# Performance work log

Hardware: AMD Instinct MI355X
Metric: run time of the kernel (lower is better)

The kernel has to match this reference:

```python
import jax, jax.numpy as jnp
import numpy as np

N, E, B, D, L = 100000, 600000, 128, 128, 3
BOT = 64
EPS = 1e-5


def _forward(query_x, corpus_x, gin_eps, mlp_W1, mlp_b1, mlp_W2, mlp_b2, bn_gamma, bn_beta,
             pool_G1, pool_g1b, pool_G2, pool_g2b, pool_Wm,
             int_G1, int_g1b, int_G2, int_g2b, int_F1, int_f1b, int_F2, int_f2b,
             sc_G1, sc_g1b, sc_G2, sc_g2b, sc_F1, sc_f1b, sc_F2, sc_f2b,
             query_edge_index, query_graph_idx, corpus_edge_index, corpus_graph_idx, num_graphs):
    def gin(x, ei, l):
        # GINConv: sum of source-node features into targets, plus (1+eps)*self
        agg = jax.ops.segment_sum(x[ei[0]], ei[1], num_segments=x.shape[0])
        h = (1.0 + gin_eps[l]) * x + agg
        h = jax.nn.relu(h @ mlp_W1[l] + mlp_b1[l]) @ mlp_W2[l] + mlp_b2[l]
        mu = h.mean(axis=0)
        var = ((h - mu) ** 2).mean(axis=0)  # biased var (BatchNorm training mode)
        h = (h - mu) * jax.lax.rsqrt(var + EPS) * bn_gamma[l] + bn_beta[l]
        return jax.nn.relu(h)  # dropout p=0.0

    def pool(x, gidx, l):
        coef = jnp.tanh(jax.nn.relu(x @ pool_G1[l] + pool_g1b[l]) @ pool_G2[l] + pool_g2b[l])
        s = (coef + 1.0) * x
        sums = jax.ops.segment_sum(s, gidx, num_segments=num_graphs)
        cnt = jax.ops.segment_sum(jnp.ones((x.shape[0],), x.dtype), gidx, num_segments=num_graphs)
        mean = sums / cnt[:, None]
        gc = jnp.tanh(mean @ pool_Wm[l])  # [B, D]
        node_coef = jax.nn.sigmoid(jnp.sum(s * gc[gidx], axis=1))  # [N]
        return jax.ops.segment_sum(node_coef[:, None] * s, gidx, num_segments=num_graphs)

    def interact(q, c, l):
        comb = jnp.concatenate([q, c], axis=1)  # [B, 2D]
        coef = jax.nn.sigmoid(jax.nn.relu(comb @ int_G1[l] + int_g1b[l]) @ int_G2[l] + int_g2b[l])
        sc = (coef + 1.0) * comb
        return jax.nn.relu(jax.nn.relu(sc @ int_F1[l] + int_f1b[l]) @ int_F2[l] + int_f2b[l])

    qx, cx = query_x, corpus_x
    feats = []
    for l in range(gin_eps.shape[0]):
        qx = gin(qx, query_edge_index, l)
        cx = gin(cx, corpus_edge_index, l)
        feats.append(interact(pool(qx, query_graph_idx, l), pool(cx, corpus_graph_idx, l), l))
    f = jnp.concatenate(feats, axis=1)  # [B, sum(filters)//2]
    coef = jax.nn.sigmoid(jax.nn.relu(f @ sc_G1 + sc_g1b) @ sc_G2 + sc_g2b)
    sf = (coef + 1.0) * f
    return (jax.nn.relu(sf @ sc_F1 + sc_f1b) @ sc_F2 + sc_f2b).squeeze(-1)  # [B]


def setup_inputs() -> dict:
    key = jax.random.key(0)
    kit = iter(jax.random.split(key, 64))
    def nrm(shape, s=0.05):
        return jax.random.normal(next(kit), shape, jnp.float32) * s
    C, R, OUT, AGG, RG = 2 * D, (2 * D) // 4, D // 2, (3 * D) // 2, ((3 * D) // 2) // 4
    inp = {
        "query_x": nrm((N, D), 1.0),
        "query_edge_index": jax.random.randint(next(kit), (2, E), 0, N),
        "query_graph_idx": jnp.sort(jax.random.randint(next(kit), (N,), 0, B)),
        "corpus_x": nrm((N, D), 1.0),
        "corpus_edge_index": jax.random.randint(next(kit), (2, E), 0, N),
        "corpus_graph_idx": jnp.sort(jax.random.randint(next(kit), (N,), 0, B)),
        "num_graphs": B,
        "gin_eps": jnp.zeros((L,), jnp.float32),
        "mlp_W1": nrm((L, D, D)), "mlp_b1": jnp.zeros((L, D)),
        "mlp_W2": nrm((L, D, D)), "mlp_b2": jnp.zeros((L, D)),
        "bn_gamma": jnp.ones((L, D)), "bn_beta": jnp.zeros((L, D)),
        "pool_G1": nrm((L, D, D // 4)), "pool_g1b": jnp.zeros((L, D // 4)),
        "pool_G2": nrm((L, D // 4, D)), "pool_g2b": jnp.zeros((L, D)),
        "pool_Wm": nrm((L, D, D)),
        "int_G1": nrm((L, C, R)), "int_g1b": jnp.zeros((L, R)),
        "int_G2": nrm((L, R, C)), "int_g2b": jnp.zeros((L, C)),
        "int_F1": nrm((L, C, C)), "int_f1b": jnp.zeros((L, C)),
        "int_F2": nrm((L, C, OUT)), "int_f2b": jnp.zeros((L, OUT)),
        "sc_G1": nrm((AGG, RG)), "sc_g1b": jnp.zeros((RG,)),
        "sc_G2": nrm((RG, AGG)), "sc_g2b": jnp.zeros((AGG,)),
        "sc_F1": nrm((AGG, BOT)), "sc_f1b": jnp.zeros((BOT,)),
        "sc_F2": nrm((BOT, 1)), "sc_f2b": jnp.zeros((1,)),
    }
    return inp


def reference(query_x, query_edge_index, query_graph_idx, corpus_x, corpus_edge_index, corpus_graph_idx,
              num_graphs, gin_eps, mlp_W1, mlp_b1, mlp_W2, mlp_b2, bn_gamma, bn_beta,
              pool_G1, pool_g1b, pool_G2, pool_g2b, pool_Wm,
              int_G1, int_g1b, int_G2, int_g2b, int_F1, int_f1b, int_F2, int_f2b,
              sc_G1, sc_g1b, sc_G2, sc_g2b, sc_F1, sc_f1b, sc_F2, sc_f2b):
    return _forward(query_x, corpus_x, gin_eps, mlp_W1, mlp_b1, mlp_W2, mlp_b2, bn_gamma, bn_beta,
                    pool_G1, pool_g1b, pool_G2, pool_g2b, pool_Wm,
                    int_G1, int_g1b, int_G2, int_g2b, int_F1, int_f1b, int_F2, int_f2b,
                    sc_G1, sc_g1b, sc_G2, sc_g2b, sc_F1, sc_f1b, sc_F2, sc_f2b,
                    query_edge_index, query_graph_idx, corpus_edge_index, corpus_graph_idx, num_graphs)
```

## Files before the change

kernel.cpp:

```cpp
#include <hip/hip_runtime.h>
#include <hip/hip_bf16.h>

constexpr int NN  = 100000;
constexpr int NN2 = 200000;
constexpr int NE  = 600000;
constexpr int NB  = 128;
constexpr int D   = 128;
constexpr int NL  = 3;
constexpr int CAP = 48;
constexpr int MT_TOT = NN2 / 16;
constexpr int MT_Q   = NN / 16;

typedef __bf16 bf16x8 __attribute__((ext_vector_type(8)));
typedef float f32x4 __attribute__((ext_vector_type(4)));
typedef unsigned short us8 __attribute__((ext_vector_type(8)));

__device__ __forceinline__ float sigmoidf_(float x) { return 1.0f / (1.0f + __expf(-x)); }
__device__ __forceinline__ unsigned short f2b(float f) {
    __hip_bfloat16 h = __float2bfloat16(f);
    return __builtin_bit_cast(unsigned short, h);
}
__device__ __forceinline__ float b2f(unsigned short u) {
    __hip_bfloat16 h = __builtin_bit_cast(__hip_bfloat16, u);
    return __bfloat162float(h);
}
__device__ __forceinline__ bf16x8 ldfrag(const unsigned short* p) {
    return __builtin_bit_cast(bf16x8, *(const us8*)p);
}

__global__ __launch_bounds__(256) void k_csr_fill(const int* __restrict__ ei, int* __restrict__ deg,
                                                  int* __restrict__ bucket, int off) {
    int e = blockIdx.x * 256 + threadIdx.x;
    if (e < NE) {
        int src = ei[e] + off;
        int dst = ei[NE + e] + off;
        int pos = atomicAdd(&deg[dst], 1);
        if (pos < CAP) bucket[(size_t)dst * CAP + pos] = src;
    }
}

__global__ __launch_bounds__(256) void k_wprep_all(
    const float* mW1, const float* mW2, const float* pG1, const float* pG2,
    const float* iG1, const float* iG2, const float* iF1, const float* iF2,
    const float* sG1, const float* sG2, const float* sF1,
    unsigned short* W1t, unsigned short* W2t, unsigned short* G1t, unsigned short* G2t,
    unsigned short* iG1t, unsigned short* iG2t, unsigned short* iF1t, unsigned short* iF2t,
    unsigned short* sG1t, unsigned short* sG2t, unsigned short* sF1t) {
    int i = blockIdx.x * 256 + threadIdx.x;
#define SEG(CNT, KK, NN_, SRC, DST)                                              \
    if (i < (CNT)) {                                                             \
        int l = i / ((KK) * (NN_)), r = i % ((KK) * (NN_));                      \
        int n = r / (KK), k = r % (KK);                                          \
        DST[i] = f2b(SRC[(size_t)l * (KK) * (NN_) + (size_t)k * (NN_) + n]);     \
        return;                                                                  \
    }                                                                            \
    i -= (CNT);
    SEG(49152, 128, 128, mW1, W1t)
    SEG(49152, 128, 128, mW2, W2t)
    SEG(12288, 128, 32, pG1, G1t)
    SEG(12288, 32, 128, pG2, G2t)
    SEG(49152, 256, 64, iG1, iG1t)
    SEG(49152, 64, 256, iG2, iG2t)
    SEG(196608, 256, 256, iF1, iF1t)
    SEG(49152, 256, 64, iF2, iF2t)
    SEG(9216, 192, 48, sG1, sG1t)
    if (i < 12288) {
        int n = i / 64, k = i % 64;
        sG2t[i] = (k < 48) ? f2b(sG2[(size_t)k * 192 + n]) : (unsigned short)0;
        return;
    }
    i -= 12288;
    SEG(12288, 192, 64, sF1, sF1t)
#undef SEG
}

template <bool BF16IN>
__global__ __launch_bounds__(256) void k_gather(const float* __restrict__ qx, const float* __restrict__ cx,
                                                const unsigned short* __restrict__ xb, unsigned short* __restrict__ z,
                                                const int* __restrict__ deg, const int* __restrict__ bucket,
                                                const float* __restrict__ eps_p, int l) {
    int r = blockIdx.x * 16 + (threadIdx.x >> 4);
    int c8 = threadIdx.x & 15;
    float e = 1.0f + eps_p[l];
    float a[8];
    const float* base = nullptr; int off = 0;
    if constexpr (BF16IN) {
        us8 v = *(const us8*)(xb + (size_t)r * D + c8 * 8);
#pragma unroll
        for (int j = 0; j < 8; ++j) a[j] = e * b2f(v[j]);
    } else {
        base = (r < NN) ? qx : cx; off = (r < NN) ? 0 : NN;
        float4 v0 = *(const float4*)(base + (size_t)(r - off) * D + c8 * 8);
        float4 v1 = *(const float4*)(base + (size_t)(r - off) * D + c8 * 8 + 4);
        a[0] = e * v0.x; a[1] = e * v0.y; a[2] = e * v0.z; a[3] = e * v0.w;
        a[4] = e * v1.x; a[5] = e * v1.y; a[6] = e * v1.z; a[7] = e * v1.w;
    }
    int d = deg[r]; d = (d < CAP) ? d : CAP;
    const int* bk = bucket + (size_t)r * CAP;
    int i = 0;
    for (; i + 4 <= d; i += 4) {
        int s0 = bk[i], s1 = bk[i + 1], s2 = bk[i + 2], s3 = bk[i + 3];
        if constexpr (BF16IN) {
            us8 u0 = *(const us8*)(xb + (size_t)s0 * D + c8 * 8);
            us8 u1 = *(const us8*)(xb + (size_t)s1 * D + c8 * 8);
            us8 u2 = *(const us8*)(xb + (size_t)s2 * D + c8 * 8);
            us8 u3 = *(const us8*)(xb + (size_t)s3 * D + c8 * 8);
#pragma unroll
            for (int j = 0; j < 8; ++j)
                a[j] += b2f(u0[j]) + b2f(u1[j]) + b2f(u2[j]) + b2f(u3[j]);
        } else {
            const float* p0 = base + (size_t)(s0 - off) * D + c8 * 8;
            const float* p1 = base + (size_t)(s1 - off) * D + c8 * 8;
            const float* p2 = base + (size_t)(s2 - off) * D + c8 * 8;
            const float* p3 = base + (size_t)(s3 - off) * D + c8 * 8;
            float4 w0 = *(const float4*)p0, w0b = *(const float4*)(p0 + 4);
            float4 w1 = *(const float4*)p1, w1b = *(const float4*)(p1 + 4);
            float4 w2 = *(const float4*)p2, w2b = *(const float4*)(p2 + 4);
            float4 w3 = *(const float4*)p3, w3b = *(const float4*)(p3 + 4);
            a[0] += w0.x + w1.x + w2.x + w3.x; a[1] += w0.y + w1.y + w2.y + w3.y;
            a[2] += w0.z + w1.z + w2.z + w3.z; a[3] += w0.w + w1.w + w2.w + w3.w;
            a[4] += w0b.x + w1b.x + w2b.x + w3b.x; a[5] += w0b.y + w1b.y + w2b.y + w3b.y;
            a[6] += w0b.z + w1b.z + w2b.z + w3b.z; a[7] += w0b.w + w1b.w + w2b.w + w3b.w;
        }
    }
    for (; i < d; ++i) {
        int s0 = bk[i];
        if constexpr (BF16IN) {
            us8 u0 = *(const us8*)(xb + (size_t)s0 * D + c8 * 8);
#pragma unroll
            for (int j = 0; j < 8; ++j) a[j] += b2f(u0[j]);
        } else {
            const float* p0 = base + (size_t)(s0 - off) * D + c8 * 8;
            float4 w0 = *(const float4*)p0, w0b = *(const float4*)(p0 + 4);
            a[0] += w0.x; a[1] += w0.y; a[2] += w0.z; a[3] += w0.w;
            a[4] += w0b.x; a[5] += w0b.y; a[6] += w0b.z; a[7] += w0b.w;
        }
    }
    us8 o;
#pragma unroll
    for (int j = 0; j < 8; ++j) o[j] = f2b(a[j]);
    *(us8*)(z + (size_t)r * D + c8 * 8) = o;
}

constexpr int HSTR = 136;
__global__ __launch_bounds__(256, 2) void k_mlp(unsigned short* zh,
                                                const unsigned short* __restrict__ W1t,
                                                const unsigned short* __restrict__ W2t,
                                                const float* __restrict__ b1,
                                                const float* __restrict__ b2,
                                                float* __restrict__ stat) {
    __shared__ unsigned short hb[2][2][16 * HSTR];
    __shared__ float red[512];
    int wave = threadIdx.x >> 6, lane = threadIdx.x & 63;
    int col16 = lane & 15, quad = lane >> 4;
    int g = wave >> 1, half = wave & 1;
    bf16x8 bf1[4][4], bf2[4][4];
    float bb1[4], bb2[4];
#pragma unroll
    for (int t = 0; t < 4; ++t) {
        int c = half * 64 + t * 16 + col16;
        bb1[t] = b1[c]; bb2[t] = b2[c];
#pragma unroll
        for (int kc = 0; kc < 4; ++kc) {
            bf1[t][kc] = ldfrag(W1t + (size_t)c * D + kc * 32 + quad * 8);
            bf2[t][kc] = ldfrag(W2t + (size_t)c * D + kc * 32 + quad * 8);
        }
    }
    float cs[2][4] = {{0.f,0.f,0.f,0.f},{0.f,0.f,0.f,0.f}};
    float cq[2][4] = {{0.f,0.f,0.f,0.f},{0.f,0.f,0.f,0.f}};
    int groups = gridDim.x * 2;
    int iters = (MT_TOT + groups - 1) / groups;
    for (int n = 0; n < iters; ++n) {
        int mt = blockIdx.x * 2 + g + n * groups;
        bool act = (mt < MT_TOT);
        int pp = n & 1;
        unsigned short* hbuf = hb[pp][g];
        {
            const unsigned short* Ap = zh + ((size_t)(act ? mt : 0) * 16 + col16) * D + quad * 8;
            f32x4 acc[4];
#pragma unroll
            for (int t = 0; t < 4; ++t) acc[t] = (f32x4){0.f, 0.f, 0.f, 0.f};
#pragma unroll
            for (int kc = 0; kc < 4; ++kc) {
                bf16x8 af = ldfrag(Ap + kc * 32);
#pragma unroll
                for (int t = 0; t < 4; ++t)
                    acc[t] = __builtin_amdgcn_mfma_f32_16x16x32_bf16(af, bf1[t][kc], acc[t], 0, 0, 0);
            }
#pragma unroll
            for (int t = 0; t < 4; ++t) {
                int c = half * 64 + t * 16 + col16;
#pragma unroll
                for (int r = 0; r < 4; ++r)
                    hbuf[(quad * 4 + r) * HSTR + c] = f2b(fmaxf(acc[t][r] + bb1[t], 0.f));
            }
        }
        __syncthreads();
        {
            f32x4 acc[4];
#pragma unroll
            for (int t = 0; t < 4; ++t) acc[t] = (f32x4){0.f, 0.f, 0.f, 0.f};
#pragma unroll
            for (int kc = 0; kc < 4; ++kc) {
                bf16x8 af = ldfrag(&hbuf[col16 * HSTR + kc * 32 + quad * 8]);
#pragma unroll
                for (int t = 0; t < 4; ++t)
                    acc[t] = __builtin_amdgcn_mfma_f32_16x16x32_bf16(af, bf2[t][kc], acc[t], 0, 0, 0);
            }
            if (act) {
                int side = (mt < MT_Q) ? 0 : 1;
#pragma unroll
                for (int t = 0; t < 4; ++t) {
                    int c = half * 64 + t * 16 + col16;
#pragma unroll
                    for (int r = 0; r < 4; ++r) {
                        int m = mt * 16 + quad * 4 + r;
                        float v = acc[t][r] + bb2[t];
                        zh[(size_t)m * D + c] = f2b(v);
                        cs[side][t] += v; cq[side][t] += v * v;
                    }
                }
            }
        }
    }
    for (int i = threadIdx.x; i < 512; i += 256) red[i] = 0.f;
    __syncthreads();
#pragma unroll
    for (int t = 0; t < 4; ++t) {
        int c = half * 64 + t * 16 + col16;
#pragma unroll
        for (int side = 0; side < 2; ++side) {
            atomicAdd(&red[side * 256 + c], cs[side][t]);
            atomicAdd(&red[side * 256 + 128 + c], cq[side][t]);
        }
    }
    __syncthreads();
    for (int i = threadIdx.x; i < 512; i += 256) atomicAdd(&stat[i], red[i]);
}

__global__ __launch_bounds__(256, 2) void k_pool(const unsigned short* __restrict__ H,
                                                 const unsigned short* __restrict__ G1t,
                                                 const unsigned short* __restrict__ G2t,
                                                 const float* __restrict__ b1,
                                                 const float* __restrict__ b2,
                                                 const float* __restrict__ stat,
                                                 const float* __restrict__ gamma,
                                                 const float* __restrict__ beta,
                                                 unsigned short* __restrict__ Xo,
                                                 unsigned short* __restrict__ S) {
    __shared__ float sc_s[256], sh_s[256];
    __shared__ unsigned short xt[4][16 * HSTR];
    __shared__ unsigned short t2t[4][16 * 40];
    {
        int t = threadIdx.x, side = t >> 7, c = t & 127;
        const float invN = 1.0f / (float)NN;
        float mu = stat[side * 256 + c] * invN;
        float var = fmaxf(stat[side * 256 + 128 + c] * invN - mu * mu, 0.f);
        float inv = rsqrtf(var + 1e-5f);
        float s = gamma[c] * inv;
        sc_s[t] = s;
        sh_s[t] = beta[c] - mu * s;
    }
    __syncthreads();
    int wave = threadIdx.x >> 6, lane = threadIdx.x & 63;
    int col16 = lane & 15, quad = lane >> 4;
    unsigned short* xtile = xt[wave];
    unsigned short* t2tile = t2t[wave];
    bf16x8 g1f[2][4], g2f[8];
    float bb1[2], bb2[8];
#pragma unroll
    for (int t = 0; t < 2; ++t) {
        int c = t * 16 + col16;
        bb1[t] = b1[c];
#pragma unroll
        for (int kc = 0; kc < 4; ++kc)
            g1f[t][kc] = ldfrag(G1t + (size_t)c * D + kc * 32 + quad * 8);
    }
#pragma unroll
    for (int t = 0; t < 8; ++t) {
        int c = t * 16 + col16;
        bb2[t] = b2[c];
        g2f[t] = ldfrag(G2t + (size_t)c * 32 + quad * 8);
    }
    for (int mt = blockIdx.x * 4 + wave; mt < MT_TOT; mt += gridDim.x * 4) {
        int side = (mt < MT_Q) ? 0 : 1;
        const float* scp = sc_s + side * 128;
        const float* shp = sh_s + side * 128;
        const unsigned short* Hp = H + ((size_t)mt * 16 + col16) * D + quad * 8;
        unsigned short* Xp = Xo + ((size_t)mt * 16 + col16) * D + quad * 8;
        f32x4 acc1[2];
#pragma unroll
        for (int t = 0; t < 2; ++t) acc1[t] = (f32x4){0.f, 0.f, 0.f, 0.f};
#pragma unroll
        for (int kc = 0; kc < 4; ++kc) {
            us8 hv = *(const us8*)(Hp + kc * 32);
            int k0 = kc * 32 + quad * 8;
            float4 s0 = *(const float4*)&scp[k0], s1 = *(const float4*)&scp[k0 + 4];
            float4 h0 = *(const float4*)&shp[k0], h1 = *(const float4*)&shp[k0 + 4];
            us8 xv;
            xv[0] = f2b(fmaxf(b2f(hv[0]) * s0.x + h0.x, 0.f));
            xv[1] = f2b(fmaxf(b2f(hv[1]) * s0.y + h0.y, 0.f));
            xv[2] = f2b(fmaxf(b2f(hv[2]) * s0.z + h0.z, 0.f));
            xv[3] = f2b(fmaxf(b2f(hv[3]) * s0.w + h0.w, 0.f));
            xv[4] = f2b(fmaxf(b2f(hv[4]) * s1.x + h1.x, 0.f));
            xv[5] = f2b(fmaxf(b2f(hv[5]) * s1.y + h1.y, 0.f));
            xv[6] = f2b(fmaxf(b2f(hv[6]) * s1.z + h1.z, 0.f));
            xv[7] = f2b(fmaxf(b2f(hv[7]) * s1.w + h1.w, 0.f));
            *(us8*)(Xp + kc * 32) = xv;
            *(us8*)(xtile + col16 * HSTR + k0) = xv;
            bf16x8 af = __builtin_bit_cast(bf16x8, xv);
#pragma unroll
            for (int t = 0; t < 2; ++t)
                acc1[t] = __builtin_amdgcn_mfma_f32_16x16x32_bf16(af, g1f[t][kc], acc1[t], 0, 0, 0);
        }
#pragma unroll
        for (int t = 0; t < 2; ++t) {
            int c = t * 16 + col16;
#pragma unroll
            for (int r = 0; r < 4; ++r)
                t2tile[(quad * 4 + r) * 40 + c] = f2b(fmaxf(acc1[t][r] + bb1[t], 0.f));
        }
        bf16x8 af2 = ldfrag(t2tile + col16 * 40 + quad * 8);
        f32x4 acc2[8];
#pragma unroll
        for (int t = 0; t < 8; ++t) {
            acc2[t] = (f32x4){0.f, 0.f, 0.f, 0.f};
            acc2[t] = __builtin_amdgcn_mfma_f32_16x16x32_bf16(af2, g2f[t], acc2[t], 0, 0, 0);
        }
#pragma unroll
        for (int t = 0; t < 8; ++t) {
            int c = t * 16 + col16;
#pragma unroll
            for (int r = 0; r < 4; ++r) {
                int mrow = quad * 4 + r;
                float v = tanhf(acc2[t][r] + bb2[t]) + 1.f;
                S[((size_t)mt * 16 + mrow) * D + c] = f2b(v * b2f(xtile[mrow * HSTR + c]));
            }
        }
    }
}

__global__ __launch_bounds__(256) void k_segsum(const unsigned short* __restrict__ S,
                                                const int* __restrict__ gq, const int* __restrict__ gc,
                                                float* __restrict__ dst, float* __restrict__ cnt) {
    int c = threadIdx.x & (D - 1);
    int sub = threadIdx.x >> 7;
    int per = (NN2 + gridDim.x - 1) / gridDim.x;
    int r0 = blockIdx.x * per;
    int r1 = min(r0 + per, NN2);
    int r = r0 + sub;
    if (r >= r1) return;
    float acc = 0.f, cn = 0.f;
    int cur = (r < NN) ? gq[r] : 128 + gc[r - NN];
    for (; r < r1; r += 2) {
        int g = (r < NN) ? gq[r] : 128 + gc[r - NN];
        if (g != cur) {
            atomicAdd(&dst[cur * D + c], acc);
            if (c == 0) atomicAdd(&cnt[cur], cn);
            acc = 0.f; cn = 0.f; cur = g;
        }
        acc += b2f(S[(size_t)r * D + c]);
        cn += 1.f;
    }
    atomicAdd(&dst[cur * D + c], acc);
    if (c == 0) atomicAdd(&cnt[cur], cn);
}

__global__ void k_gc(const float* __restrict__ sums, const float* __restrict__ cnt,
                     const float* __restrict__ Wm, float* __restrict__ gc) {
    __shared__ float m[D];
    int b = blockIdx.x, j = threadIdx.x;
    m[j] = sums[b * D + j] / cnt[b];
    __syncthreads();
    float a = 0.f;
#pragma unroll 8
    for (int i = 0; i < D; ++i) a += m[i] * Wm[i * D + j];
    gc[b * D + j] = tanhf(a);
}

__global__ __launch_bounds__(256) void k_ncseg(const unsigned short* __restrict__ S,
                                               const int* __restrict__ gq, const int* __restrict__ gc,
                                               const float* __restrict__ gcb,
                                               float* __restrict__ dq, float* __restrict__ dc) {
    int stream = blockIdx.x * 4 + (threadIdx.x >> 6);
    int lane = threadIdx.x & 63;
    int nstream = gridDim.x * 4;
    int per = (NN2 + nstream - 1) / nstream;
    int r0 = stream * per;
    int r1 = min(r0 + per, NN2);
    if (r0 >= r1) return;
    float a0 = 0.f, a1 = 0.f;
    int cur = (r0 < NN) ? gq[r0] : 128 + gc[r0 - NN];
    for (int r = r0; r < r1; ++r) {
        int g = (r < NN) ? gq[r] : 128 + gc[r - NN];
        if (g != cur) {
            float* base = (cur < 128) ? (dq + cur * D) : (dc + (cur - 128) * D);
            atomicAdd(&base[lane * 2], a0);
            atomicAdd(&base[lane * 2 + 1], a1);
            a0 = 0.f; a1 = 0.f; cur = g;
        }
        ushort2 sv = *(const ushort2*)&S[(size_t)r * D + lane * 2];
        float2 gv = *(const float2*)&gcb[(size_t)g * D + lane * 2];
        float v0 = b2f(sv.x), v1 = b2f(sv.y);
        float p = v0 * gv.x + v1 * gv.y;
#pragma unroll
        for (int off = 1; off < 64; off <<= 1) p += __shfl_xor(p, off, 64);
        float nc = sigmoidf_(p);
        a0 += nc * v0; a1 += nc * v1;
    }
    float* base = (cur < 128) ? (dq + cur * D) : (dc + (cur - 128) * D);
    atomicAdd(&base[lane * 2], a0);
    atomicAdd(&base[lane * 2 + 1], a1);
}

constexpr int LSTR = 264;
__global__ __launch_bounds__(256) void k_interact(const float* __restrict__ pooled,
                                                  const unsigned short* __restrict__ iG1t, const float* __restrict__ ig1b,
                                                  const unsigned short* __restrict__ iG2t, const float* __restrict__ ig2b,
                                                  const unsigned short* __restrict__ iF1t, const float* __restrict__ if1b,
                                                  const unsigned short* __restrict__ iF2t, const float* __restrict__ if2b,
                                                  unsigned short* __restrict__ featsb) {
    __shared__ unsigned short bufC[16 * LSTR];
    __shared__ unsigned short bufA[16 * LSTR];
    __shared__ unsigned short bufB[16 * LSTR];
    int t = threadIdx.x, wave = t >> 6, lane = t & 63;
    int col16 = lane & 15, quad = lane >> 4;
    int pg = blockIdx.x & 7, l = blockIdx.x >> 3;
    int p0 = pg * 16;
    {
        int r = t >> 4, c0 = (t & 15) * 16;
        const float* src = (c0 < 128)
            ? (pooled + (size_t)l * NB * D + (size_t)(p0 + r) * D + c0)
            : (pooled + (size_t)(NL + l) * NB * D + (size_t)(p0 + r) * D + (c0 - 128));
#pragma unroll
        for (int j = 0; j < 16; ++j) bufC[r * LSTR + c0 + j] = f2b(src[j]);
    }
    __syncthreads();
    {
        f32x4 acc = (f32x4){0.f, 0.f, 0.f, 0.f};
        int n = wave * 16 + col16;
#pragma unroll
        for (int kc = 0; kc < 8; ++kc) {
            bf16x8 af = ldfrag(&bufC[col16 * LSTR + kc * 32 + quad * 8]);
            bf16x8 bfr = ldfrag(iG1t + ((size_t)l * 64 + n) * 256 + kc * 32 + quad * 8);
            acc = __builtin_amdgcn_mfma_f32_16x16x32_bf16(af, bfr, acc, 0, 0, 0);
        }
        float bb = ig1b[(size_t)l * 64 + n];
#pragma unroll
// ... 116 lines not shown
            bf16x8 af = ldfrag(&bufA[col16 * LSTR + kc * 32 + quad * 8]);
#pragma unroll
            for (int tt = 0; tt < 3; ++tt) {
                int n = wave * 48 + tt * 16 + col16;
                bf16x8 bfr = ldfrag(sG2t + (size_t)n * 64 + kc * 32 + quad * 8);
                acc[tt] = __builtin_amdgcn_mfma_f32_16x16x32_bf16(af, bfr, acc[tt], 0, 0, 0);
            }
        }
#pragma unroll
        for (int tt = 0; tt < 3; ++tt) {
            int n = wave * 48 + tt * 16 + col16;
            float bb = sg2b[n];
#pragma unroll
            for (int r = 0; r < 4; ++r) {
                int row = quad * 4 + r;
                float s = (sigmoidf_(acc[tt][r] + bb) + 1.f) * b2f(bufF[row * 200 + n]);
                bufB[row * LSTR + n] = f2b(s);
            }
        }
    }
    __syncthreads();
    {
        f32x4 acc = (f32x4){0.f, 0.f, 0.f, 0.f};
        int n = wave * 16 + col16;
#pragma unroll
        for (int kc = 0; kc < 6; ++kc) {
            bf16x8 af = ldfrag(&bufB[col16 * LSTR + kc * 32 + quad * 8]);
            bf16x8 bfr = ldfrag(sF1t + (size_t)n * 192 + kc * 32 + quad * 8);
            acc = __builtin_amdgcn_mfma_f32_16x16x32_bf16(af, bfr, acc, 0, 0, 0);
        }
        float bb = sf1b[n], w2 = sF2[n];
#pragma unroll
        for (int r = 0; r < 4; ++r)
            redf[(quad * 4 + r) * 65 + n] = fmaxf(acc[r] + bb, 0.f) * w2;
    }
    __syncthreads();
    if (t < 16) {
        float s = 0.f;
#pragma unroll 8
        for (int i = 0; i < 64; ++i) s += redf[t * 65 + i];
        out[p0 + t] = s + sf2b[0];
    }
}

extern "C" void kernel_launch(void* const* d_in, const int* in_sizes, int n_in,
                              void* d_out, int out_size, void* d_ws, size_t ws_size,
                              hipStream_t stream) {
    const float* query_x   = (const float*)d_in[0];
    const int*   query_ei  = (const int*)d_in[1];
    const int*   query_gi  = (const int*)d_in[2];
    const float* corpus_x  = (const float*)d_in[3];
    const int*   corpus_ei = (const int*)d_in[4];
    const int*   corpus_gi = (const int*)d_in[5];
    const float* gin_eps   = (const float*)d_in[7];
    const float* mlp_W1    = (const float*)d_in[8];
    const float* mlp_b1    = (const float*)d_in[9];
    const float* mlp_W2    = (const float*)d_in[10];
    const float* mlp_b2    = (const float*)d_in[11];
    const float* bn_gamma  = (const float*)d_in[12];
    const float* bn_beta   = (const float*)d_in[13];
    const float* pool_G1   = (const float*)d_in[14];
    const float* pool_g1b  = (const float*)d_in[15];
    const float* pool_G2   = (const float*)d_in[16];
    const float* pool_g2b  = (const float*)d_in[17];
    const float* pool_Wm   = (const float*)d_in[18];
    const float* int_G1    = (const float*)d_in[19];
    const float* int_g1b   = (const float*)d_in[20];
    const float* int_G2    = (const float*)d_in[21];
    const float* int_g2b   = (const float*)d_in[22];
    const float* int_F1    = (const float*)d_in[23];
    const float* int_f1b   = (const float*)d_in[24];
    const float* int_F2    = (const float*)d_in[25];
    const float* int_f2b   = (const float*)d_in[26];
    const float* sc_G1     = (const float*)d_in[27];
    const float* sc_g1b    = (const float*)d_in[28];
    const float* sc_G2     = (const float*)d_in[29];
    const float* sc_g2b    = (const float*)d_in[30];
    const float* sc_F1     = (const float*)d_in[31];
    const float* sc_f1b    = (const float*)d_in[32];
    const float* sc_F2     = (const float*)d_in[33];
    const float* sc_f2b    = (const float*)d_in[34];
    float* out = (float*)d_out;

    unsigned short* Zb  = (unsigned short*)d_ws;
    unsigned short* Xb  = Zb + (size_t)NN2 * D;
    unsigned short* Sb  = Xb + (size_t)NN2 * D;
    unsigned short* featsb = Sb + (size_t)NN2 * D;
    unsigned short* W1t = featsb + 128 * 192;
    unsigned short* W2t = W1t + NL * D * D;
    unsigned short* G1t = W2t + NL * D * D;
    unsigned short* G2t = G1t + NL * 32 * D;
    unsigned short* iG1t = G2t + NL * D * 32;
    unsigned short* iG2t = iG1t + NL * 64 * 256;
    unsigned short* iF1t = iG2t + NL * 256 * 64;
    unsigned short* iF2t = iF1t + NL * 256 * 256;
    unsigned short* sG1t = iF2t + NL * 64 * 256;
    unsigned short* sG2t = sG1t + 48 * 192;
    unsigned short* sF1t = sG2t + 192 * 64;
    int* deg    = (int*)(sF1t + 64 * 192);
    int* bucket = deg + NN2;
    float* bn_stat  = (float*)(bucket + (size_t)NN2 * CAP);
    float* seg_sum  = bn_stat + NL * 512;
    float* seg_cnt  = seg_sum + 256 * D;
    float* gcb      = seg_cnt + 256;
    float* pooled   = gcb + 256 * D;

    k_wprep_all<<<1956, 256, 0, stream>>>(mlp_W1, mlp_W2, pool_G1, pool_G2,
                                          int_G1, int_G2, int_F1, int_F2,
                                          sc_G1, sc_G2, sc_F1,
                                          W1t, W2t, G1t, G2t, iG1t, iG2t, iF1t, iF2t,
                                          sG1t, sG2t, sF1t);

    hipMemsetAsync(deg, 0, NN2 * sizeof(int), stream);
    hipMemsetAsync(bn_stat, 0, NL * 512 * sizeof(float), stream);
    hipMemsetAsync(pooled, 0, 2 * NL * NB * D * sizeof(float), stream);
    k_csr_fill<<<(NE + 255) / 256, 256, 0, stream>>>(query_ei, deg, bucket, 0);
    k_csr_fill<<<(NE + 255) / 256, 256, 0, stream>>>(corpus_ei, deg, bucket, NN);

    for (int l = 0; l < NL; ++l) {
        if (l == 0)
            k_gather<false><<<NN2 / 16, 256, 0, stream>>>(query_x, corpus_x, nullptr, Zb,
                                                          deg, bucket, gin_eps, l);
        else
            k_gather<true><<<NN2 / 16, 256, 0, stream>>>(nullptr, nullptr, Xb, Zb,
                                                         deg, bucket, gin_eps, l);
        k_mlp<<<1024, 256, 0, stream>>>(Zb, W1t + (size_t)l * D * D, W2t + (size_t)l * D * D,
                                        mlp_b1 + l * D, mlp_b2 + l * D, bn_stat + l * 512);
        k_pool<<<1024, 256, 0, stream>>>(Zb, G1t + (size_t)l * 32 * D, G2t + (size_t)l * D * 32,
                                         pool_g1b + l * 32, pool_g2b + l * D,
                                         bn_stat + l * 512, bn_gamma + l * D, bn_beta + l * D,
                                         Xb, Sb);
        hipMemsetAsync(seg_sum, 0, (256 * D + 256) * sizeof(float), stream);
        k_segsum<<<2048, 256, 0, stream>>>(Sb, query_gi, corpus_gi, seg_sum, seg_cnt);
        k_gc<<<256, D, 0, stream>>>(seg_sum, seg_cnt, pool_Wm + (size_t)l * D * D, gcb);
        k_ncseg<<<1024, 256, 0, stream>>>(Sb, query_gi, corpus_gi, gcb,
                                          pooled + (size_t)l * NB * D,
                                          pooled + (size_t)(NL + l) * NB * D);
    }
    k_interact<<<24, 256, 0, stream>>>(pooled, iG1t, int_g1b, iG2t, int_g2b,
                                       iF1t, int_f1b, iF2t, int_f2b, featsb);
    k_score<<<8, 256, 0, stream>>>(featsb, sG1t, sc_g1b, sG2t, sc_g2b,
                                   sF1t, sc_f1b, sc_F2, sc_f2b, out);
}
```

Before: 1.079 ms.

## Fuse neighbor gather into GIN MLP kernel and merge CSR fill launches

The separate gather kernel and MLP kernel are merged into one kernel. Each wave gathers a 16-row tile of neighbor sums straight into registers in MFMA A-fragment layout and then runs both 128x128 GEMMs, with no round trip of the aggregated tile through global memory. Weight fragments are now loaded from global or L2 inside the loop instead of being held in registers. The two CSR fill launches are also combined into a single launch. The fused kernel adds register pressure (32 accumulators plus 8 MFMA tiles) and changes the gather access pattern, which may lower occupancy or memory-level parallelism.

```diff
diff --git a/kernel.cpp b/kernel.cpp
--- a/kernel.cpp
+++ b/kernel.cpp
@@ -28,15 +28,17 @@
     return __builtin_bit_cast(bf16x8, *(const us8*)p);
 }
 
-__global__ __launch_bounds__(256) void k_csr_fill(const int* __restrict__ ei, int* __restrict__ deg,
-                                                  int* __restrict__ bucket, int off) {
+__global__ __launch_bounds__(256) void k_csr_fill(const int* __restrict__ qei, const int* __restrict__ cei,
+                                                  int* __restrict__ deg, int* __restrict__ bucket) {
     int e = blockIdx.x * 256 + threadIdx.x;
+    int src, dst;
     if (e < NE) {
-        int src = ei[e] + off;
-        int dst = ei[NE + e] + off;
-        int pos = atomicAdd(&deg[dst], 1);
-        if (pos < CAP) bucket[(size_t)dst * CAP + pos] = src;
-    }
+        src = qei[e]; dst = qei[NE + e];
+    } else if (e < 2 * NE) {
+        src = cei[e - NE] + NN; dst = cei[NE + (e - NE)] + NN;
+    } else return;
+    int pos = atomicAdd(&deg[dst], 1);
+    if (pos < CAP) bucket[(size_t)dst * CAP + pos] = src;
 }
 
 __global__ __launch_bounds__(256) void k_wprep_all(
@@ -74,160 +76,157 @@
 #undef SEG
 }
 
+constexpr int HSTR = 136;
 template <bool BF16IN>
-__global__ __launch_bounds__(256) void k_gather(const float* __restrict__ qx, const float* __restrict__ cx,
-                                                const unsigned short* __restrict__ xb, unsigned short* __restrict__ z,
-                                                const int* __restrict__ deg, const int* __restrict__ bucket,
-                                                const float* __restrict__ eps_p, int l) {
-    int r = blockIdx.x * 16 + (threadIdx.x >> 4);
-    int c8 = threadIdx.x & 15;
-    float e = 1.0f + eps_p[l];
-    float a[8];
-    const float* base = nullptr; int off = 0;
-    if constexpr (BF16IN) {
-        us8 v = *(const us8*)(xb + (size_t)r * D + c8 * 8);
-#pragma unroll
-        for (int j = 0; j < 8; ++j) a[j] = e * b2f(v[j]);
-    } else {
-        base = (r < NN) ? qx : cx; off = (r < NN) ? 0 : NN;
-        float4 v0 = *(const float4*)(base + (size_t)(r - off) * D + c8 * 8);
-        float4 v1 = *(const float4*)(base + (size_t)(r - off) * D + c8 * 8 + 4);
-        a[0] = e * v0.x; a[1] = e * v0.y; a[2] = e * v0.z; a[3] = e * v0.w;
-        a[4] = e * v1.x; a[5] = e * v1.y; a[6] = e * v1.z; a[7] = e * v1.w;
-    }
-    int d = deg[r]; d = (d < CAP) ? d : CAP;
-    const int* bk = bucket + (size_t)r * CAP;
-    int i = 0;
-    for (; i + 4 <= d; i += 4) {
-        int s0 = bk[i], s1 = bk[i + 1], s2 = bk[i + 2], s3 = bk[i + 3];
-        if constexpr (BF16IN) {
-            us8 u0 = *(const us8*)(xb + (size_t)s0 * D + c8 * 8);
-            us8 u1 = *(const us8*)(xb + (size_t)s1 * D + c8 * 8);
-            us8 u2 = *(const us8*)(xb + (size_t)s2 * D + c8 * 8);
-            us8 u3 = *(const us8*)(xb + (size_t)s3 * D + c8 * 8);
-#pragma unroll
-            for (int j = 0; j < 8; ++j)
-                a[j] += b2f(u0[j]) + b2f(u1[j]) + b2f(u2[j]) + b2f(u3[j]);
-        } else {
-            const float* p0 = base + (size_t)(s0 - off) * D + c8 * 8;
-            const float* p1 = base + (size_t)(s1 - off) * D + c8 * 8;
-            const float* p2 = base + (size_t)(s2 - off) * D + c8 * 8;
-            const float* p3 = base + (size_t)(s3 - off) * D + c8 * 8;
-            float4 w0 = *(const float4*)p0, w0b = *(const float4*)(p0 + 4);
-            float4 w1 = *(const float4*)p1, w1b = *(const float4*)(p1 + 4);
-            float4 w2 = *(const float4*)p2, w2b = *(const float4*)(p2 + 4);
-            float4 w3 = *(const float4*)p3, w3b = *(const float4*)(p3 + 4);
-            a[0] += w0.x + w1.x + w2.x + w3.x; a[1] += w0.y + w1.y + w2.y + w3.y;
-            a[2] += w0.z + w1.z + w2.z + w3.z; a[3] += w0.w + w1.w + w2.w + w3.w;
-            a[4] += w0b.x + w1b.x + w2b.x + w3b.x; a[5] += w0b.y + w1b.y + w2b.y + w3b.y;
-            a[6] += w0b.z + w1b.z + w2b.z + w3b.z; a[7] += w0b.w + w1b.w + w2b.w + w3b.w;
-        }
-    }
-    for (; i < d; ++i) {
-        int s0 = bk[i];
-        if constexpr (BF16IN) {
-            us8 u0 = *(const us8*)(xb + (size_t)s0 * D + c8 * 8);
-#pragma unroll
-            for (int j = 0; j < 8; ++j) a[j] += b2f(u0[j]);
-        } else {
-            const float* p0 = base + (size_t)(s0 - off) * D + c8 * 8;
-            float4 w0 = *(const float4*)p0, w0b = *(const float4*)(p0 + 4);
-            a[0] += w0.x; a[1] += w0.y; a[2] += w0.z; a[3] += w0.w;
-            a[4] += w0b.x; a[5] += w0b.y; a[6] += w0b.z; a[7] += w0b.w;
-        }
-    }
-    us8 o;
-#pragma unroll
-    for (int j = 0; j < 8; ++j) o[j] = f2b(a[j]);
-    *(us8*)(z + (size_t)r * D + c8 * 8) = o;
-}
-
-constexpr int HSTR = 136;
-__global__ __launch_bounds__(256, 2) void k_mlp(unsigned short* zh,
-                                                const unsigned short* __restrict__ W1t,
-                                                const unsigned short* __restrict__ W2t,
-                                                const float* __restrict__ b1,
-                                                const float* __restrict__ b2,
-                                                float* __restrict__ stat) {
-    __shared__ unsigned short hb[2][2][16 * HSTR];
+__global__ __launch_bounds__(256, 2) void k_gmlp(const float* __restrict__ qx, const float* __restrict__ cx,
+                                                 const unsigned short* __restrict__ Xin,
+                                                 const int* __restrict__ deg, const int* __restrict__ bucket,
+                                                 const unsigned short* __restrict__ W1t,
+                                                 const unsigned short* __restrict__ W2t,
+                                                 const float* __restrict__ b1, const float* __restrict__ b2,
+                                                 const float* __restrict__ eps_p, int l,
+                                                 unsigned short* __restrict__ H, float* __restrict__ stat) {
+    __shared__ unsigned short h1b[4][16 * HSTR];
     __shared__ float red[512];
     int wave = threadIdx.x >> 6, lane = threadIdx.x & 63;
     int col16 = lane & 15, quad = lane >> 4;
-    int g = wave >> 1, half = wave & 1;
-    bf16x8 bf1[4][4], bf2[4][4];
-    float bb1[4], bb2[4];
-#pragma unroll
-    for (int t = 0; t < 4; ++t) {
-        int c = half * 64 + t * 16 + col16;
-        bb1[t] = b1[c]; bb2[t] = b2[c];
-#pragma unroll
-        for (int kc = 0; kc < 4; ++kc) {
-            bf1[t][kc] = ldfrag(W1t + (size_t)c * D + kc * 32 + quad * 8);
-            bf2[t][kc] = ldfrag(W2t + (size_t)c * D + kc * 32 + quad * 8);
-        }
-    }
-    float cs[2][4] = {{0.f,0.f,0.f,0.f},{0.f,0.f,0.f,0.f}};
-    float cq[2][4] = {{0.f,0.f,0.f,0.f},{0.f,0.f,0.f,0.f}};
-    int groups = gridDim.x * 2;
-    int iters = (MT_TOT + groups - 1) / groups;
-    for (int n = 0; n < iters; ++n) {
-        int mt = blockIdx.x * 2 + g + n * groups;
-        bool act = (mt < MT_TOT);
-        int pp = n & 1;
-        unsigned short* hbuf = hb[pp][g];
+    unsigned short* hbuf = h1b[wave];
+    float e = 1.0f + eps_p[l];
+    float bb1[8], bb2[8];
+#pragma unroll
+    for (int t = 0; t < 8; ++t) {
+        bb1[t] = b1[t * 16 + col16];
+        bb2[t] = b2[t * 16 + col16];
+    }
+    float cs[2][8] = {{0}}, cq[2][8] = {{0}};
+
+    for (int mt = blockIdx.x * 4 + wave; mt < MT_TOT; mt += gridDim.x * 4) {
+        int r = mt * 16 + col16;
+        float a[32];
+        if constexpr (BF16IN) {
+#pragma unroll
+            for (int kc = 0; kc < 4; ++kc) {
+                us8 v = *(const us8*)(Xin + (size_t)r * D + kc * 32 + quad * 8);
+#pragma unroll
+                for (int j = 0; j < 8; ++j) a[kc * 8 + j] = e * b2f(v[j]);
+            }
+        } else {
+            const float* base = (r < NN) ? qx : cx;
+            int off = (r < NN) ? 0 : NN;
+#pragma unroll
+            for (int kc = 0; kc < 4; ++kc) {
+                const float* p = base + (size_t)(r - off) * D + kc * 32 + quad * 8;
+                float4 v0 = *(const float4*)p, v1 = *(const float4*)(p + 4);
+                a[kc * 8 + 0] = e * v0.x; a[kc * 8 + 1] = e * v0.y;
+                a[kc * 8 + 2] = e * v0.z; a[kc * 8 + 3] = e * v0.w;
+                a[kc * 8 + 4] = e * v1.x; a[kc * 8 + 5] = e * v1.y;
+                a[kc * 8 + 6] = e * v1.z; a[kc * 8 + 7] = e * v1.w;
+            }
+        }
+        int d = deg[r]; d = (d < CAP) ? d : CAP;
+        const int* bk = bucket + (size_t)r * CAP;
+        if constexpr (BF16IN) {
+            int i = 0;
+            for (; i + 2 <= d; i += 2) {
+                const unsigned short* p0 = Xin + (size_t)bk[i] * D + quad * 8;
+                const unsigned short* p1 = Xin + (size_t)bk[i + 1] * D + quad * 8;
+                us8 u0[4], u1[4];
+#pragma unroll
+                for (int kc = 0; kc < 4; ++kc) {
+                    u0[kc] = *(const us8*)(p0 + kc * 32);
+                    u1[kc] = *(const us8*)(p1 + kc * 32);
+                }
+#pragma unroll
+                for (int kc = 0; kc < 4; ++kc)
+#pragma unroll
+                    for (int j = 0; j < 8; ++j)
+                        a[kc * 8 + j] += b2f(u0[kc][j]) + b2f(u1[kc][j]);
+            }
+            if (i < d) {
+                const unsigned short* p0 = Xin + (size_t)bk[i] * D + quad * 8;
+#pragma unroll
+                for (int kc = 0; kc < 4; ++kc) {
+                    us8 u0 = *(const us8*)(p0 + kc * 32);
+#pragma unroll
+                    for (int j = 0; j < 8; ++j) a[kc * 8 + j] += b2f(u0[j]);
+                }
+            }
+        } else {
+            const float* base = (r < NN) ? qx : cx;
+            int off = (r < NN) ? 0 : NN;
+            for (int i = 0; i < d; ++i) {
+                const float* p0 = base + (size_t)(bk[i] - off) * D + quad * 8;
+                float4 w[8];
+#pragma unroll
+                for (int kc = 0; kc < 4; ++kc) {
+                    w[kc * 2] = *(const float4*)(p0 + kc * 32);
+                    w[kc * 2 + 1] = *(const float4*)(p0 + kc * 32 + 4);
+                }
+#pragma unroll
+                for (int kc = 0; kc < 4; ++kc) {
+                    a[kc * 8 + 0] += w[kc * 2].x; a[kc * 8 + 1] += w[kc * 2].y;
+                    a[kc * 8 + 2] += w[kc * 2].z; a[kc * 8 + 3] += w[kc * 2].w;
+                    a[kc * 8 + 4] += w[kc * 2 + 1].x; a[kc * 8 + 5] += w[kc * 2 + 1].y;
+                    a[kc * 8 + 6] += w[kc * 2 + 1].z; a[kc * 8 + 7] += w[kc * 2 + 1].w;
+                }
+            }
+        }
+        us8 af[4];
+#pragma unroll
+        for (int kc = 0; kc < 4; ++kc)
+#pragma unroll
+            for (int j = 0; j < 8; ++j) af[kc][j] = f2b(a[kc * 8 + j]);
         {
-            const unsigned short* Ap = zh + ((size_t)(act ? mt : 0) * 16 + col16) * D + quad * 8;
-            f32x4 acc[4];
-#pragma unroll
-            for (int t = 0; t < 4; ++t) acc[t] = (f32x4){0.f, 0.f, 0.f, 0.f};
+            f32x4 acc[8];
+#pragma unroll
+            for (int t = 0; t < 8; ++t) acc[t] = (f32x4){0.f, 0.f, 0.f, 0.f};
 #pragma unroll
             for (int kc = 0; kc < 4; ++kc) {
-                bf16x8 af = ldfrag(Ap + kc * 32);
-#pragma unroll
-                for (int t = 0; t < 4; ++t)
-                    acc[t] = __builtin_amdgcn_mfma_f32_16x16x32_bf16(af, bf1[t][kc], acc[t], 0, 0, 0);
-            }
-#pragma unroll
-            for (int t = 0; t < 4; ++t) {
-                int c = half * 64 + t * 16 + col16;
-#pragma unroll
-                for (int r = 0; r < 4; ++r)
-                    hbuf[(quad * 4 + r) * HSTR + c] = f2b(fmaxf(acc[t][r] + bb1[t], 0.f));
-            }
-        }
-        __syncthreads();
+                bf16x8 A = __builtin_bit_cast(bf16x8, af[kc]);
+#pragma unroll
+                for (int t = 0; t < 8; ++t) {
+                    bf16x8 B = ldfrag(W1t + (size_t)(t * 16 + col16) * D + kc * 32 + quad * 8);
+                    acc[t] = __builtin_amdgcn_mfma_f32_16x16x32_bf16(A, B, acc[t], 0, 0, 0);
+                }
+            }
+#pragma unroll
+            for (int t = 0; t < 8; ++t)
+#pragma unroll
+                for (int r4 = 0; r4 < 4; ++r4)
+                    hbuf[(quad * 4 + r4) * HSTR + t * 16 + col16] = f2b(fmaxf(acc[t][r4] + bb1[t], 0.f));
+        }
         {
-            f32x4 acc[4];
-#pragma unroll
-            for (int t = 0; t < 4; ++t) acc[t] = (f32x4){0.f, 0.f, 0.f, 0.f};
+            f32x4 acc[8];
+#pragma unroll
+            for (int t = 0; t < 8; ++t) acc[t] = (f32x4){0.f, 0.f, 0.f, 0.f};
 #pragma unroll
             for (int kc = 0; kc < 4; ++kc) {
-                bf16x8 af = ldfrag(&hbuf[col16 * HSTR + kc * 32 + quad * 8]);
-#pragma unroll
-                for (int t = 0; t < 4; ++t)
-                    acc[t] = __builtin_amdgcn_mfma_f32_16x16x32_bf16(af, bf2[t][kc], acc[t], 0, 0, 0);
-            }
-            if (act) {
-                int side = (mt < MT_Q) ? 0 : 1;
-#pragma unroll
-                for (int t = 0; t < 4; ++t) {
-                    int c = half * 64 + t * 16 + col16;
-#pragma unroll
-                    for (int r = 0; r < 4; ++r) {
-                        int m = mt * 16 + quad * 4 + r;
-                        float v = acc[t][r] + bb2[t];
-                        zh[(size_t)m * D + c] = f2b(v);
-                        cs[side][t] += v; cq[side][t] += v * v;
-                    }
+                bf16x8 A = __builtin_bit_cast(bf16x8, *(const us8*)&hbuf[col16 * HSTR + kc * 32 + quad * 8]);
+#pragma unroll
+                for (int t = 0; t < 8; ++t) {
+                    bf16x8 B = ldfrag(W2t + (size_t)(t * 16 + col16) * D + kc * 32 + quad * 8);
+                    acc[t] = __builtin_amdgcn_mfma_f32_16x16x32_bf16(A, B, acc[t], 0, 0, 0);
                 }
             }
+            int side = (mt < MT_Q) ? 0 : 1;
+#pragma unroll
+            for (int t = 0; t < 8; ++t) {
+                int c = t * 16 + col16;
+#pragma unroll
+                for (int r4 = 0; r4 < 4; ++r4) {
+                    int m = mt * 16 + quad * 4 + r4;
+                    float v = acc[t][r4] + bb2[t];
+                    H[(size_t)m * D + c] = f2b(v);
+                    cs[side][t] += v; cq[side][t] += v * v;
+                }
+            }
         }
     }
     for (int i = threadIdx.x; i < 512; i += 256) red[i] = 0.f;
     __syncthreads();
 #pragma unroll
-    for (int t = 0; t < 4; ++t) {
-        int c = half * 64 + t * 16 + col16;
+    for (int t = 0; t < 8; ++t) {
+        int c = t * 16 + col16;
 #pragma unroll
         for (int side = 0; side < 2; ++side) {
             atomicAdd(&red[side * 256 + c], cs[side][t]);
@@ -646,9 +645,9 @@
     const float* sc_f2b    = (const float*)d_in[34];
     float* out = (float*)d_out;
 
-    unsigned short* Zb  = (unsigned short*)d_ws;
-    unsigned short* Xb  = Zb + (size_t)NN2 * D;
-    unsigned short* Sb  = Xb + (size_t)NN2 * D;
+    unsigned short* Xb  = (unsigned short*)d_ws;
+    unsigned short* Hb  = Xb + (size_t)NN2 * D;
+    unsigned short* Sb  = Hb + (size_t)NN2 * D;
     unsigned short* featsb = Sb + (size_t)NN2 * D;
     unsigned short* W1t = featsb + 128 * 192;
     unsigned short* W2t = W1t + NL * D * D;
@@ -678,19 +677,20 @@
     hipMemsetAsync(deg, 0, NN2 * sizeof(int), stream);
     hipMemsetAsync(bn_stat, 0, NL * 512 * sizeof(float), stream);
     hipMemsetAsync(pooled, 0, 2 * NL * NB * D * sizeof(float), stream);
-    k_csr_fill<<<(NE + 255) / 256, 256, 0, stream>>>(query_ei, deg, bucket, 0);
-    k_csr_fill<<<(NE + 255) / 256, 256, 0, stream>>>(corpus_ei, deg, bucket, NN);
+    k_csr_fill<<<(2 * NE + 255) / 256, 256, 0, stream>>>(query_ei, corpus_ei, deg, bucket);
 
     for (int l = 0; l < NL; ++l) {
         if (l == 0)
-            k_gather<false><<<NN2 / 16, 256, 0, stream>>>(query_x, corpus_x, nullptr, Zb,
-                                                          deg, bucket, gin_eps, l);
+            k_gmlp<false><<<1024, 256, 0, stream>>>(query_x, corpus_x, nullptr, deg, bucket,
+                                                    W1t + (size_t)l * D * D, W2t + (size_t)l * D * D,
+                                                    mlp_b1 + l * D, mlp_b2 + l * D, gin_eps, l,
+                                                    Hb, bn_stat + l * 512);
         else
-            k_gather<true><<<NN2 / 16, 256, 0, stream>>>(nullptr, nullptr, Xb, Zb,
-                                                         deg, bucket, gin_eps, l);
-        k_mlp<<<1024, 256, 0, stream>>>(Zb, W1t + (size_t)l * D * D, W2t + (size_t)l * D * D,
-                                        mlp_b1 + l * D, mlp_b2 + l * D, bn_stat + l * 512);
-        k_pool<<<1024, 256, 0, stream>>>(Zb, G1t + (size_t)l * 32 * D, G2t + (size_t)l * D * 32,
+            k_gmlp<true><<<1024, 256, 0, stream>>>(nullptr, nullptr, Xb, deg, bucket,
+                                                   W1t + (size_t)l * D * D, W2t + (size_t)l * D * D,
+                                                   mlp_b1 + l * D, mlp_b2 + l * D, gin_eps, l,
+                                                   Hb, bn_stat + l * 512);
+        k_pool<<<1024, 256, 0, stream>>>(Hb, G1t + (size_t)l * 32 * D, G2t + (size_t)l * D * 32,
                                          pool_g1b + l * 32, pool_g2b + l * D,
                                          bn_stat + l * 512, bn_gamma + l * D, bn_beta + l * D,
                                          Xb, Sb);
```

Result: slower. 1.550 ms (+43.7%).

## Fuse per-graph segment sum into pool kernel and hoist node counts

Applied to the files above, without the earlier changes.

The pool kernel now gives each wave a contiguous range of row tiles and keeps running per-graph column sums in registers. It flushes them to seg_sum with atomics whenever the graph id changes, so the separate segsum kernel and its re-read of S each layer go away. Node counts per graph are computed once by a new count kernel instead of every layer, and the two CSR fill launches are merged into one. The cost is extra per-row graph-index loads inside pool and a smaller grid (782 blocks) with contiguous ranges, which may hurt load balance.

```diff
diff --git a/kernel.cpp b/kernel.cpp
--- a/kernel.cpp
+++ b/kernel.cpp
@@ -28,15 +28,41 @@
     return __builtin_bit_cast(bf16x8, *(const us8*)p);
 }
 
-__global__ __launch_bounds__(256) void k_csr_fill(const int* __restrict__ ei, int* __restrict__ deg,
-                                                  int* __restrict__ bucket, int off) {
+__global__ __launch_bounds__(256) void k_csr_fill(const int* __restrict__ qei, const int* __restrict__ cei,
+                                                  int* __restrict__ deg, int* __restrict__ bucket) {
     int e = blockIdx.x * 256 + threadIdx.x;
+    int src, dst;
     if (e < NE) {
-        int src = ei[e] + off;
-        int dst = ei[NE + e] + off;
-        int pos = atomicAdd(&deg[dst], 1);
-        if (pos < CAP) bucket[(size_t)dst * CAP + pos] = src;
-    }
+        src = qei[e]; dst = qei[NE + e];
+    } else if (e < 2 * NE) {
+        src = cei[e - NE] + NN; dst = cei[NE + (e - NE)] + NN;
+    } else return;
+    int pos = atomicAdd(&deg[dst], 1);
+    if (pos < CAP) bucket[(size_t)dst * CAP + pos] = src;
+}
+
+__global__ __launch_bounds__(256) void k_cnt(const int* __restrict__ gq, const int* __restrict__ gc,
+                                             float* __restrict__ cnt) {
+    __shared__ float h[256];
+    for (int i = threadIdx.x; i < 256; i += 256) h[i] = 0.f;
+    __syncthreads();
+    int total = gridDim.x * 256;
+    int tid = blockIdx.x * 256 + threadIdx.x;
+    int per = (NN2 + total - 1) / total;
+    int r0 = tid * per, r1 = min(r0 + per, NN2);
+    if (r0 < r1) {
+        int cur = (r0 < NN) ? gq[r0] : 128 + gc[r0 - NN];
+        float c = 0.f;
+        for (int r = r0; r < r1; ++r) {
+            int g = (r < NN) ? gq[r] : 128 + gc[r - NN];
+            if (g != cur) { atomicAdd(&h[cur], c); c = 0.f; cur = g; }
+            c += 1.f;
+        }
+        atomicAdd(&h[cur], c);
+    }
+    __syncthreads();
+    for (int i = threadIdx.x; i < 256; i += 256)
+        if (h[i] != 0.f) atomicAdd(&cnt[i], h[i]);
 }
 
 __global__ __launch_bounds__(256) void k_wprep_all(
@@ -246,8 +272,10 @@
                                                  const float* __restrict__ stat,
                                                  const float* __restrict__ gamma,
                                                  const float* __restrict__ beta,
+                                                 const int* __restrict__ gq, const int* __restrict__ gcix,
                                                  unsigned short* __restrict__ Xo,
-                                                 unsigned short* __restrict__ S) {
+                                                 unsigned short* __restrict__ S,
+                                                 float* __restrict__ seg_sum) {
     __shared__ float sc_s[256], sh_s[256];
     __shared__ unsigned short xt[4][16 * HSTR];
     __shared__ unsigned short t2t[4][16 * 40];
@@ -266,6 +294,12 @@
     int col16 = lane & 15, quad = lane >> 4;
     unsigned short* xtile = xt[wave];
     unsigned short* t2tile = t2t[wave];
+    int nwaves = gridDim.x * 4;
+    int per = (MT_TOT + nwaves - 1) / nwaves;
+    int wid = blockIdx.x * 4 + wave;
+    int mt0 = wid * per, mt1 = min(mt0 + per, MT_TOT);
+    if (mt0 >= mt1) return;
+
     bf16x8 g1f[2][4], g2f[8];
     float bb1[2], bb2[8];
 #pragma unroll
@@ -282,7 +316,9 @@
         bb2[t] = b2[c];
         g2f[t] = ldfrag(G2t + (size_t)c * 32 + quad * 8);
     }
-    for (int mt = blockIdx.x * 4 + wave; mt < MT_TOT; mt += gridDim.x * 4) {
+    float sacc[8] = {0.f, 0.f, 0.f, 0.f, 0.f, 0.f, 0.f, 0.f};
+    int curg = -1;
+    for (int mt = mt0; mt < mt1; ++mt) {
         int side = (mt < MT_Q) ? 0 : 1;
         const float* scp = sc_s + side * 128;
         const float* shp = sh_s + side * 128;
@@ -328,42 +364,33 @@
             acc2[t] = __builtin_amdgcn_mfma_f32_16x16x32_bf16(af2, g2f[t], acc2[t], 0, 0, 0);
         }
 #pragma unroll
-        for (int t = 0; t < 8; ++t) {
-            int c = t * 16 + col16;
-#pragma unroll
-            for (int r = 0; r < 4; ++r) {
-                int mrow = quad * 4 + r;
-                float v = tanhf(acc2[t][r] + bb2[t]) + 1.f;
-                S[((size_t)mt * 16 + mrow) * D + c] = f2b(v * b2f(xtile[mrow * HSTR + c]));
-            }
-        }
-    }
-}
-
-__global__ __launch_bounds__(256) void k_segsum(const unsigned short* __restrict__ S,
-                                                const int* __restrict__ gq, const int* __restrict__ gc,
-                                                float* __restrict__ dst, float* __restrict__ cnt) {
-    int c = threadIdx.x & (D - 1);
-    int sub = threadIdx.x >> 7;
-    int per = (NN2 + gridDim.x - 1) / gridDim.x;
-    int r0 = blockIdx.x * per;
-    int r1 = min(r0 + per, NN2);
-    int r = r0 + sub;
-    if (r >= r1) return;
-    float acc = 0.f, cn = 0.f;
-    int cur = (r < NN) ? gq[r] : 128 + gc[r - NN];
-    for (; r < r1; r += 2) {
-        int g = (r < NN) ? gq[r] : 128 + gc[r - NN];
-        if (g != cur) {
-            atomicAdd(&dst[cur * D + c], acc);
-            if (c == 0) atomicAdd(&cnt[cur], cn);
-            acc = 0.f; cn = 0.f; cur = g;
-        }
-        acc += b2f(S[(size_t)r * D + c]);
-        cn += 1.f;
-    }
-    atomicAdd(&dst[cur * D + c], acc);
-    if (c == 0) atomicAdd(&cnt[cur], cn);
+        for (int r = 0; r < 4; ++r) {
+            int m = mt * 16 + quad * 4 + r;
+            int g = (m < NN) ? gq[m] : 128 + gcix[m - NN];
+            if (g != curg) {
+                if (curg >= 0) {
+#pragma unroll
+                    for (int t = 0; t < 8; ++t) {
+                        atomicAdd(&seg_sum[(size_t)curg * D + t * 16 + col16], sacc[t]);
+                        sacc[t] = 0.f;
+                    }
+                }
+                curg = g;
+            }
+#pragma unroll
+            for (int t = 0; t < 8; ++t) {
+                int c = t * 16 + col16;
+                float v = (tanhf(acc2[t][r] + bb2[t]) + 1.f) * b2f(xtile[(quad * 4 + r) * HSTR + c]);
+                S[(size_t)m * D + c] = f2b(v);
+                sacc[t] += v;
+            }
+        }
+    }
+    if (curg >= 0) {
+#pragma unroll
+        for (int t = 0; t < 8; ++t)
+            atomicAdd(&seg_sum[(size_t)curg * D + t * 16 + col16], sacc[t]);
+    }
 }
 
 __global__ void k_gc(const float* __restrict__ sums, const float* __restrict__ cnt,
@@ -678,8 +705,9 @@
     hipMemsetAsync(deg, 0, NN2 * sizeof(int), stream);
     hipMemsetAsync(bn_stat, 0, NL * 512 * sizeof(float), stream);
     hipMemsetAsync(pooled, 0, 2 * NL * NB * D * sizeof(float), stream);
-    k_csr_fill<<<(NE + 255) / 256, 256, 0, stream>>>(query_ei, deg, bucket, 0);
-    k_csr_fill<<<(NE + 255) / 256, 256, 0, stream>>>(corpus_ei, deg, bucket, NN);
+    hipMemsetAsync(seg_cnt, 0, 256 * sizeof(float), stream);
+    k_csr_fill<<<(2 * NE + 255) / 256, 256, 0, stream>>>(query_ei, corpus_ei, deg, bucket);
+    k_cnt<<<64, 256, 0, stream>>>(query_gi, corpus_gi, seg_cnt);
 
     for (int l = 0; l < NL; ++l) {
         if (l == 0)
@@ -690,12 +718,11 @@
                                                          deg, bucket, gin_eps, l);
         k_mlp<<<1024, 256, 0, stream>>>(Zb, W1t + (size_t)l * D * D, W2t + (size_t)l * D * D,
                                         mlp_b1 + l * D, mlp_b2 + l * D, bn_stat + l * 512);
-        k_pool<<<1024, 256, 0, stream>>>(Zb, G1t + (size_t)l * 32 * D, G2t + (size_t)l * D * 32,
-                                         pool_g1b + l * 32, pool_g2b + l * D,
-                                         bn_stat + l * 512, bn_gamma + l * D, bn_beta + l * D,
-                                         Xb, Sb);
-        hipMemsetAsync(seg_sum, 0, (256 * D + 256) * sizeof(float), stream);
-        k_segsum<<<2048, 256, 0, stream>>>(Sb, query_gi, corpus_gi, seg_sum, seg_cnt);
+        hipMemsetAsync(seg_sum, 0, 256 * D * sizeof(float), stream);
+        k_pool<<<782, 256, 0, stream>>>(Zb, G1t + (size_t)l * 32 * D, G2t + (size_t)l * D * 32,
+                                        pool_g1b + l * 32, pool_g2b + l * D,
+                                        bn_stat + l * 512, bn_gamma + l * D, bn_beta + l * D,
+                                        query_gi, corpus_gi, Xb, Sb, seg_sum);
         k_gc<<<256, D, 0, stream>>>(seg_sum, seg_cnt, pool_Wm + (size_t)l * D * D, gcb);
         k_ncseg<<<1024, 256, 0, stream>>>(Sb, query_gi, corpus_gi, gcb,
                                           pooled + (size_t)l * NB * D,
```

Result: no change. 1.075 ms (-0.3%).
